# Kernel tuning notes

Measured on AMD Instinct MI355X. Metric: run time of the kernel, lower is better.

Reference implementation:

```python
import jax, jax.numpy as jnp
import numpy as np


def setup_inputs() -> dict:
    key = jax.random.key(0)
    k1, k2, k3, k4 = jax.random.split(key, 4)
    B, N, D, P = 1, 8192, 128, 2  # batch must be 1 (see .view(B,N,N) in source)
    x = jax.random.normal(k1, (B, N, D), dtype=jnp.float32)
    points = jax.random.normal(k2, (B, N, P), dtype=jnp.float32)
    # nn.Linear params, stored as (in, out) so y = x @ W + b
    W1 = jax.random.normal(k3, (2 * D, 2 * D), dtype=jnp.float32) * 0.04
    b1 = jnp.zeros((2 * D,), dtype=jnp.float32)
    W2 = jax.random.normal(k4, (2 * D, D), dtype=jnp.float32) * 0.04
    b2 = jnp.zeros((D,), dtype=jnp.float32)
    return {"x": x, "points": points, "W1": W1, "b1": b1, "W2": W2, "b2": b2, "K": 16}


def reference(x, points, W1, b1, W2, b2, K):
    B, N, _ = points.shape
    D = x.shape[-1]
    # torch.cdist on flattened (B*N, P) points, reshaped to (B, N, N)
    # (valid only for B == 1, matching the original module). Squared distance
    # is monotone in Euclidean distance, so top-k indices are identical.
    pf = points.reshape(B * N, -1)
    sq = jnp.sum(pf * pf, axis=-1)
    d2 = sq[:, None] + sq[None, :] - 2.0 * (pf @ pf.T)  # (BN, BN)
    d2 = d2.reshape(B, N, N)
    # topk(-dist, K+1) -> nearest K+1 (self first), drop self
    _, idx = jax.lax.top_k(-d2, K + 1)  # (B, N, K+1)
    idx = idx[:, :, 1:]  # (B, N, K)
    # gather neighbor features: knn_fts[b, n, k] = x[b, idx[b, n, k]]
    knn = x[jnp.arange(B)[:, None, None], idx]  # (B, N, K, D)
    center = jnp.broadcast_to(x[:, :, None, :], (B, N, K, D))
    local = jnp.concatenate([knn - center, center], axis=-1)  # (B, N, K, 2D)
    h = jax.nn.gelu(local @ W1 + b1, approximate=False)
    h = jax.nn.gelu(h @ W2 + b2, approximate=False)
    return jnp.mean(h, axis=2)  # (B, N, D)
```

## Files before the change

kernel.cpp:

```cpp
#include <hip/hip_runtime.h>

typedef __attribute__((ext_vector_type(8))) short short8;
typedef __attribute__((ext_vector_type(4))) float f32x4;

__device__ __forceinline__ unsigned short f2bf(float f) {
    unsigned int u = __float_as_uint(f);
    unsigned int r = u + 0x7fffu + ((u >> 16) & 1u);
    return (unsigned short)(r >> 16);
}

__device__ __forceinline__ float bf2f(short s) {
    return __uint_as_float(((unsigned int)(unsigned short)s) << 16);
}

__device__ __forceinline__ float gelu_fast(float v) {
    float x2 = v * v;
    float s  = v * fmaf(-0.102943195f, x2, -2.3022077f);
    float e  = __builtin_amdgcn_exp2f(s);
    return v * __builtin_amdgcn_rcpf(1.0f + e);
}

__device__ __forceinline__ unsigned int d2key(float d2) {
    unsigned int u = __float_as_uint(d2);
    return u ^ (((unsigned int)(((int)u) >> 31)) | 0x80000000u);
}

#define U64MAX 0xFFFFFFFFFFFFFFFFull

#define D2_FROM_Q(px, py, XI, YI, SQI)                                           \
    ({ const float sqj_ = __fadd_rn(__fmul_rn((px), (px)), __fmul_rn((py), (py))); \
       const float t_   = fmaf((YI), (py), __fmul_rn((XI), (px)));                 \
       const float s_   = __fadd_rn((SQI), sqj_);                                  \
       fmaf(-2.0f, t_, s_); })

__device__ __forceinline__ unsigned long long bitonic64(unsigned long long v, int lane) {
#pragma unroll
    for (int k = 2; k <= 64; k <<= 1) {
#pragma unroll
        for (int j = k >> 1; j > 0; j >>= 1) {
            unsigned long long pv = __shfl_xor(v, j, 64);
            const bool up  = ((lane & k) == 0);
            const bool low = ((lane & j) == 0);
            const unsigned long long mn = (v < pv) ? v : pv;
            const unsigned long long mx = (v < pv) ? pv : v;
            v = (up == low) ? mn : mx;
        }
    }
    return v;
}

__device__ __forceinline__ float bitonic64f(float v, int lane) {
#pragma unroll
    for (int k = 2; k <= 64; k <<= 1) {
#pragma unroll
        for (int j = k >> 1; j > 0; j >>= 1) {
            float pv = __shfl_xor(v, j, 64);
            const bool up  = ((lane & k) == 0);
            const bool low = ((lane & j) == 0);
            const float mn = fminf(v, pv);
            const float mx = fmaxf(v, pv);
            v = (up == low) ? mn : mx;
        }
    }
    return v;
}

__device__ __forceinline__ void insert_cand(
        unsigned long long* crow, int* cnt,
        float px, float py, float XI, float YI, float SQI, int i) {
    const float d2 = D2_FROM_Q(px, py, XI, YI, SQI);
    const unsigned int key = d2key(d2);
    int pos = atomicAdd(cnt, 1);
    if (pos < 128)
        crow[pos] = ((unsigned long long)key << 32) | (unsigned int)i;
}

#define KNN_SLACK 2.0e-3f

__global__ __launch_bounds__(512) void knn_kernel(
        const float* __restrict__ points,
        const float* __restrict__ W1, const float* __restrict__ W2,
        unsigned short* __restrict__ W1t, unsigned short* __restrict__ W2t,
        int* __restrict__ idx_out) {
    __shared__ float pmin[8][8][64];
    __shared__ float tshr[8];
    __shared__ unsigned long long cand[8][128];
    __shared__ int ccnt[8];

    const int bid = blockIdx.x;
    const int tid = threadIdx.x;

    if (bid < 192) {
        int g = bid * 512 + tid;
        if (g < 65536) {
            int d = g >> 8, c = g & 255;
            W1t[c * 256 + d] = f2bf(W1[g]);
        } else {
            int g2 = g - 65536;
            int d = g2 >> 7, c = g2 & 127;
            W2t[c * 256 + d] = f2bf(W2[g2]);
        }
        return;
    }

    const int wv    = tid >> 6;
    const int lane  = tid & 63;
    const int qbase = (bid - 192) << 3;

    float xi[8], yi[8], sqi_[8], n2x[8], n2y[8];
#pragma unroll
    for (int t = 0; t < 8; ++t) {
        xi[t] = points[(qbase + t) * 2 + 0];
        yi[t] = points[(qbase + t) * 2 + 1];
        sqi_[t] = __fadd_rn(__fmul_rn(xi[t], xi[t]), __fmul_rn(yi[t], yi[t]));
        n2x[t] = -2.0f * xi[t];
        n2y[t] = -2.0f * yi[t];
    }

    const float4* p4 = (const float4*)points;
    const float4* pw = p4 + wv * 512 + lane;

    if (tid < 8) ccnt[tid] = 0;

    float vmn[8] = {1e30f, 1e30f, 1e30f, 1e30f, 1e30f, 1e30f, 1e30f, 1e30f};
#pragma unroll
    for (int j = 0; j < 8; ++j) {
        const float4 pp = pw[j * 64];
        const float sqa = fmaf(pp.x, pp.x, pp.y * pp.y);
        const float sqb = fmaf(pp.z, pp.z, pp.w * pp.w);
#pragma unroll
        for (int t = 0; t < 8; ++t) {
            const float da = fmaf(n2x[t], pp.x, fmaf(n2y[t], pp.y, sqa));
            const float db = fmaf(n2x[t], pp.z, fmaf(n2y[t], pp.w, sqb));
            vmn[t] = fminf(fminf(da, db), vmn[t]);
        }
    }
#pragma unroll
    for (int t = 0; t < 8; ++t) pmin[t][wv][lane] = vmn[t];
    __syncthreads();

    {
        float m = pmin[wv][0][lane];
#pragma unroll
        for (int w = 1; w < 8; ++w) m = fminf(m, pmin[wv][w][lane]);
        const float s = bitonic64f(m, lane);
        if (lane == 16) tshr[wv] = s + KNN_SLACK;
    }
    __syncthreads();
    float Ta[8];
#pragma unroll
    for (int t = 0; t < 8; ++t) Ta[t] = tshr[t];

#pragma unroll
    for (int j = 0; j < 8; ++j) {
        const float4 pp = pw[j * 64];
        const int i0 = (wv * 512 + j * 64 + lane) * 2;
        const float sqa = fmaf(pp.x, pp.x, pp.y * pp.y);
        const float sqb = fmaf(pp.z, pp.z, pp.w * pp.w);
#pragma unroll
        for (int t = 0; t < 8; ++t) {
            const float da = fmaf(n2x[t], pp.x, fmaf(n2y[t], pp.y, sqa));
            const float db = fmaf(n2x[t], pp.z, fmaf(n2y[t], pp.w, sqb));
            if (da <= Ta[t])
                insert_cand(cand[t], &ccnt[t],
                            pp.x, pp.y, xi[t], yi[t], sqi_[t], i0);
            if (db <= Ta[t])
                insert_cand(cand[t], &ccnt[t],
                            pp.z, pp.w, xi[t], yi[t], sqi_[t], i0 + 1);
        }
    }
    __syncthreads();

    {
        const int q = qbase + wv;
        unsigned long long* candw = cand[wv];
        const int cc = ccnt[wv];
        const int n = cc < 128 ? cc : 128;
        if (n <= 64) {
            unsigned long long v0 = (lane < n) ? candw[lane] : U64MAX;
            v0 = bitonic64(v0, lane);
            if (lane >= 1 && lane <= 16)
                idx_out[q * 16 + lane - 1] = (int)(unsigned int)(v0 & 0xFFFFFFFFull);
        } else {
            unsigned long long v0 = (lane < n)      ? candw[lane]      : U64MAX;
            unsigned long long v1 = (lane + 64 < n) ? candw[lane + 64] : U64MAX;
#pragma unroll 1
            for (int pick = 0; pick < 17; ++pick) {
                unsigned long long m = (v0 < v1) ? v0 : v1;
#pragma unroll
                for (int d = 1; d < 64; d <<= 1) {
                    unsigned long long pm = __shfl_xor(m, d, 64);
                    m = (pm < m) ? pm : m;
                }
                if (pick > 0 && lane == 0)
                    idx_out[q * 16 + pick - 1] = (int)(unsigned int)(m & 0xFFFFFFFFull);
                if (v0 == m) v0 = U64MAX;
                else if (v1 == m) v1 = U64MAX;
            }
        }
    }
}

__global__ __launch_bounds__(256) void gemmAD_kernel(
        const float* __restrict__ x, const unsigned short* __restrict__ W1t,
        const float* __restrict__ b1,
        unsigned short* __restrict__ Abf, unsigned short* __restrict__ Dbf) {
    __shared__ unsigned short sx[64 * 136];
    __shared__ unsigned short tA[64 * 68];
    __shared__ unsigned short tD[64 * 68];
    const int tid = threadIdx.x;
    const int rb  = (blockIdx.x >> 2) * 64;
    const int cb  = (blockIdx.x & 3) * 64;

    {
        const int r   = ((tid >> 6) << 4) | (tid & 15);
        const int seg = (tid >> 4) & 3;
        const float* xr = x + (rb + r) * 128 + seg * 32;
        unsigned short* dst = sx + r * 136 + seg * 32;
#pragma unroll
        for (int u = 0; u < 8; ++u) {
            float4 a = ((const float4*)xr)[u];
            uint2 w;
            w.x = (unsigned)f2bf(a.x) | ((unsigned)f2bf(a.y) << 16);
            w.y = (unsigned)f2bf(a.z) | ((unsigned)f2bf(a.w) << 16);
            *(uint2*)(dst + u * 4) = w;
        }
    }
    __syncthreads();

    const int lane = tid & 63, wv = tid >> 6;
    const int m = lane & 15, quad = lane >> 4;
    const int ko0 = quad * 8;

    f32x4 accA[4], accC[4];
#pragma unroll
    for (int i = 0; i < 4; ++i) { accA[i] = (f32x4){0,0,0,0}; accC[i] = (f32x4){0,0,0,0}; }

    const int colL = wv * 16 + m;

#pragma unroll
    for (int ks = 0; ks < 4; ++ks) {
        const int ko = ks * 32 + ko0;
        short8 af[4];
#pragma unroll
        for (int rt = 0; rt < 4; ++rt)
            af[rt] = *(const short8*)(sx + (rt * 16 + m) * 136 + ko);
        const unsigned short* wp = W1t + (cb + colL) * 256 + ko;
        const short8 bA = *(const short8*)(wp);
        const short8 bC = *(const short8*)(wp + 128);
#pragma unroll
        for (int rt = 0; rt < 4; ++rt) {
            accA[rt] = __builtin_amdgcn_mfma_f32_16x16x32_bf16(af[rt], bA, accA[rt], 0, 0, 0);
            accC[rt] = __builtin_amdgcn_mfma_f32_16x16x32_bf16(af[rt], bC, accC[rt], 0, 0, 0);
        }
    }

    {
        const float bias = b1[cb + colL];
#pragma unroll
        for (int rt = 0; rt < 4; ++rt)
#pragma unroll
            for (int j = 0; j < 4; ++j) {
                const int rowL = rt * 16 + quad * 4 + j;
                float a = accA[rt][j];
                float d = accC[rt][j] - a + bias;
                tA[rowL * 68 + colL] = f2bf(a);
                tD[rowL * 68 + colL] = f2bf(d);
            }
    }
    __syncthreads();

    {
        const int r  = tid >> 2;
        const int sg = tid & 3;
        const unsigned short* sa = tA + r * 68 + sg * 16;
        const unsigned short* sd = tD + r * 68 + sg * 16;
        unsigned short* da = Abf + (rb + r) * 256 + cb + sg * 16;
        unsigned short* dd = Dbf + (rb + r) * 256 + cb + sg * 16;
        *(short8*)(da)     = *(const short8*)(sa);
        *(short8*)(da + 8) = *(const short8*)(sa + 8);
        *(short8*)(dd)     = *(const short8*)(sd);
        *(short8*)(dd + 8) = *(const short8*)(sd + 8);
    }
}

__global__ __launch_bounds__(256) void mlp_kernel(
        const unsigned short* __restrict__ Abf, const unsigned short* __restrict__ Dbf,
        const unsigned short* __restrict__ W2t, const float* __restrict__ b2,
        const int* __restrict__ idx, float* __restrict__ out) {
    __shared__ unsigned short sh[64 * 264];
    const int tid = threadIdx.x;
    const int qb  = blockIdx.x << 2;

    {
        const int r   = ((tid >> 6) << 4) | (tid & 15);
        const int seg = (tid >> 4) & 3;
        const int gq  = qb + (r >> 4);
        const int nb  = idx[(gq << 4) + (r & 15)];
        const unsigned short* arow = Abf + nb * 256 + seg * 64;
        const unsigned short* drow = Dbf + gq * 256 + seg * 64;
        unsigned short* dst = sh + r * 264 + seg * 64;
#pragma unroll
        for (int u = 0; u < 8; ++u) {
            short8 av = *(const short8*)(arow + u * 8);
            short8 dv = *(const short8*)(drow + u * 8);
            short8 hv;
#pragma unroll
            for (int e = 0; e < 8; ++e) {
                float h = bf2f(av[e]) + bf2f(dv[e]);
                hv[e] = (short)f2bf(gelu_fast(h));
            }
            *(short8*)(dst + u * 8) = hv;
        }
    }
    __syncthreads();

    const int lane = tid & 63, wv = tid >> 6;
    const int m = lane & 15, quad = lane >> 4;
    const int ko0 = quad * 8;

    f32x4 acc2[8];
#pragma unroll
    for (int i = 0; i < 8; ++i) acc2[i] = (f32x4){0.f, 0.f, 0.f, 0.f};
#pragma unroll
    for (int ks = 0; ks < 8; ++ks) {
        const int ko = ks * 32 + ko0;
        short8 af[4], bfr[2];
#pragma unroll
        for (int rt = 0; rt < 4; ++rt)
            af[rt] = *(const short8*)(sh + (rt * 16 + m) * 264 + ko);
#pragma unroll
        for (int ct = 0; ct < 2; ++ct)
            bfr[ct] = *(const short8*)(W2t + (wv * 32 + ct * 16 + m) * 256 + ko);
#pragma unroll
        for (int rt = 0; rt < 4; ++rt)
#pragma unroll
            for (int ct = 0; ct < 2; ++ct)
                acc2[rt * 2 + ct] = __builtin_amdgcn_mfma_f32_16x16x32_bf16(
                    af[rt], bfr[ct], acc2[rt * 2 + ct], 0, 0, 0);
    }

#pragma unroll
    for (int ct = 0; ct < 2; ++ct) {
        const int col = wv * 32 + ct * 16 + m;
        const float bias = b2[col];
#pragma unroll
        for (int rt = 0; rt < 4; ++rt) {
            float s = 0.f;
#pragma unroll
            for (int j = 0; j < 4; ++j)
                s += gelu_fast(acc2[rt * 2 + ct][j] + bias);
            s += __shfl_xor(s, 16, 64);
            s += __shfl_xor(s, 32, 64);
            if (quad == 0) out[(qb + rt) * 128 + col] = s * 0.0625f;
        }
    }
}

extern "C" void kernel_launch(void* const* d_in, const int* in_sizes, int n_in,
                              void* d_out, int out_size, void* d_ws, size_t ws_size,
                              hipStream_t stream) {
    const float* x      = (const float*)d_in[0];
    const float* points = (const float*)d_in[1];
    const float* W1     = (const float*)d_in[2];
    const float* b1     = (const float*)d_in[3];
    const float* W2     = (const float*)d_in[4];
    const float* b2     = (const float*)d_in[5];
    float* out = (float*)d_out;

    char* ws = (char*)d_ws;
    unsigned short* W1t = (unsigned short*)ws;
    unsigned short* W2t = (unsigned short*)(ws + 131072);
    int*            idx = (int*)(ws + 196608);
    unsigned short* Abf = (unsigned short*)(ws + 720896);
    unsigned short* Dbf = (unsigned short*)(ws + 4915200);

    knn_kernel<<<1216, 512, 0, stream>>>(points, W1, W2, W1t, W2t, idx);
    gemmAD_kernel<<<512, 256, 0, stream>>>(x, W1t, b1, Abf, Dbf);
    mlp_kernel<<<2048, 256, 0, stream>>>(Abf, Dbf, W2t, b2, idx, out);
}
```

Before: 135.6 us.

## Shrink kNN blocks to four queries, use packed FMA, convert W1 in gemm

Measured after the change: 138.0 us. No clear change (+1.8%).

```diff
diff --git a/kernel.cpp b/kernel.cpp
--- a/kernel.cpp
+++ b/kernel.cpp
@@ -2,6 +2,7 @@
 
 typedef __attribute__((ext_vector_type(8))) short short8;
 typedef __attribute__((ext_vector_type(4))) float f32x4;
+typedef __attribute__((ext_vector_type(2))) float f32x2;
 
 __device__ __forceinline__ unsigned short f2bf(float f) {
     unsigned int u = __float_as_uint(f);
@@ -23,6 +24,17 @@
 __device__ __forceinline__ unsigned int d2key(float d2) {
     unsigned int u = __float_as_uint(d2);
     return u ^ (((unsigned int)(((int)u) >> 31)) | 0x80000000u);
+}
+
+__device__ __forceinline__ f32x2 pk_fma(f32x2 a, f32x2 b, f32x2 c) {
+    f32x2 d;
+    asm("v_pk_fma_f32 %0, %1, %2, %3" : "=v"(d) : "v"(a), "v"(b), "v"(c));
+    return d;
+}
+__device__ __forceinline__ f32x2 pk_mul(f32x2 a, f32x2 b) {
+    f32x2 d;
+    asm("v_pk_mul_f32 %0, %1, %2" : "=v"(d) : "v"(a), "v"(b));
+    return d;
 }
 
 #define U64MAX 0xFFFFFFFFFFFFFFFFull
@@ -77,94 +89,88 @@
 
 #define KNN_SLACK 2.0e-3f
 
-__global__ __launch_bounds__(512) void knn_kernel(
+__global__ __launch_bounds__(256) void knn_kernel(
         const float* __restrict__ points,
-        const float* __restrict__ W1, const float* __restrict__ W2,
-        unsigned short* __restrict__ W1t, unsigned short* __restrict__ W2t,
+        const float* __restrict__ W2,
+        unsigned short* __restrict__ W2t,
         int* __restrict__ idx_out) {
-    __shared__ float pmin[8][8][64];
-    __shared__ float tshr[8];
-    __shared__ unsigned long long cand[8][128];
-    __shared__ int ccnt[8];
+    __shared__ float pmin[4][4][64];
+    __shared__ float tshr[4];
+    __shared__ unsigned long long cand[4][128];
+    __shared__ int ccnt[4];
 
     const int bid = blockIdx.x;
     const int tid = threadIdx.x;
 
-    if (bid < 192) {
-        int g = bid * 512 + tid;
-        if (g < 65536) {
-            int d = g >> 8, c = g & 255;
-            W1t[c * 256 + d] = f2bf(W1[g]);
-        } else {
-            int g2 = g - 65536;
-            int d = g2 >> 7, c = g2 & 127;
-            W2t[c * 256 + d] = f2bf(W2[g2]);
-        }
+    if (bid < 128) {
+        int g = bid * 256 + tid;
+        int d = g >> 7, c = g & 127;
+        W2t[c * 256 + d] = f2bf(W2[g]);
         return;
     }
 
     const int wv    = tid >> 6;
     const int lane  = tid & 63;
-    const int qbase = (bid - 192) << 3;
-
-    float xi[8], yi[8], sqi_[8], n2x[8], n2y[8];
-#pragma unroll
-    for (int t = 0; t < 8; ++t) {
+    const int qbase = (bid - 128) << 2;
+
+    float xi[4], yi[4], sqi_[4];
+    f32x2 n2x2[4], n2y2[4];
+#pragma unroll
+    for (int t = 0; t < 4; ++t) {
         xi[t] = points[(qbase + t) * 2 + 0];
         yi[t] = points[(qbase + t) * 2 + 1];
         sqi_[t] = __fadd_rn(__fmul_rn(xi[t], xi[t]), __fmul_rn(yi[t], yi[t]));
-        n2x[t] = -2.0f * xi[t];
-        n2y[t] = -2.0f * yi[t];
+        const float nx = -2.0f * xi[t], ny = -2.0f * yi[t];
+        n2x2[t] = (f32x2){nx, nx};
+        n2y2[t] = (f32x2){ny, ny};
     }
 
     const float4* p4 = (const float4*)points;
-    const float4* pw = p4 + wv * 512 + lane;
-
-    if (tid < 8) ccnt[tid] = 0;
-
-    float vmn[8] = {1e30f, 1e30f, 1e30f, 1e30f, 1e30f, 1e30f, 1e30f, 1e30f};
-#pragma unroll
-    for (int j = 0; j < 8; ++j) {
+    const float4* pw = p4 + wv * 1024 + lane;
+
+    if (tid < 4) ccnt[tid] = 0;
+
+    float vmn[4] = {1e30f, 1e30f, 1e30f, 1e30f};
+#pragma unroll 4
+    for (int j = 0; j < 16; ++j) {
         const float4 pp = pw[j * 64];
-        const float sqa = fmaf(pp.x, pp.x, pp.y * pp.y);
-        const float sqb = fmaf(pp.z, pp.z, pp.w * pp.w);
-#pragma unroll
-        for (int t = 0; t < 8; ++t) {
-            const float da = fmaf(n2x[t], pp.x, fmaf(n2y[t], pp.y, sqa));
-            const float db = fmaf(n2x[t], pp.z, fmaf(n2y[t], pp.w, sqb));
-            vmn[t] = fminf(fminf(da, db), vmn[t]);
-        }
-    }
-#pragma unroll
-    for (int t = 0; t < 8; ++t) pmin[t][wv][lane] = vmn[t];
-    __syncthreads();
-
-    {
-        float m = pmin[wv][0][lane];
-#pragma unroll
-        for (int w = 1; w < 8; ++w) m = fminf(m, pmin[wv][w][lane]);
+        const f32x2 pxz = {pp.x, pp.z}, pyw = {pp.y, pp.w};
+        const f32x2 sq2 = pk_fma(pxz, pxz, pk_mul(pyw, pyw));
+#pragma unroll
+        for (int t = 0; t < 4; ++t) {
+            const f32x2 d2 = pk_fma(n2x2[t], pxz, pk_fma(n2y2[t], pyw, sq2));
+            vmn[t] = fminf(fminf(d2.x, d2.y), vmn[t]);
+        }
+    }
+#pragma unroll
+    for (int t = 0; t < 4; ++t) pmin[t][wv][lane] = vmn[t];
+    __syncthreads();
+
+    {
+        const int q = wv;
+        const float m = fminf(fminf(pmin[q][0][lane], pmin[q][1][lane]),
+                              fminf(pmin[q][2][lane], pmin[q][3][lane]));
         const float s = bitonic64f(m, lane);
-        if (lane == 16) tshr[wv] = s + KNN_SLACK;
-    }
-    __syncthreads();
-    float Ta[8];
-#pragma unroll
-    for (int t = 0; t < 8; ++t) Ta[t] = tshr[t];
-
-#pragma unroll
-    for (int j = 0; j < 8; ++j) {
+        if (lane == 16) tshr[q] = s + KNN_SLACK;
+    }
+    __syncthreads();
+    float Ta[4];
+#pragma unroll
+    for (int t = 0; t < 4; ++t) Ta[t] = tshr[t];
+
+#pragma unroll 4
+    for (int j = 0; j < 16; ++j) {
         const float4 pp = pw[j * 64];
-        const int i0 = (wv * 512 + j * 64 + lane) * 2;
-        const float sqa = fmaf(pp.x, pp.x, pp.y * pp.y);
-        const float sqb = fmaf(pp.z, pp.z, pp.w * pp.w);
-#pragma unroll
-        for (int t = 0; t < 8; ++t) {
-            const float da = fmaf(n2x[t], pp.x, fmaf(n2y[t], pp.y, sqa));
-            const float db = fmaf(n2x[t], pp.z, fmaf(n2y[t], pp.w, sqb));
-            if (da <= Ta[t])
+        const int i0 = (wv * 1024 + j * 64 + lane) * 2;
+        const f32x2 pxz = {pp.x, pp.z}, pyw = {pp.y, pp.w};
+        const f32x2 sq2 = pk_fma(pxz, pxz, pk_mul(pyw, pyw));
+#pragma unroll
+        for (int t = 0; t < 4; ++t) {
+            const f32x2 d2 = pk_fma(n2x2[t], pxz, pk_fma(n2y2[t], pyw, sq2));
+            if (d2.x <= Ta[t])
                 insert_cand(cand[t], &ccnt[t],
                             pp.x, pp.y, xi[t], yi[t], sqi_[t], i0);
-            if (db <= Ta[t])
+            if (d2.y <= Ta[t])
                 insert_cand(cand[t], &ccnt[t],
                             pp.z, pp.w, xi[t], yi[t], sqi_[t], i0 + 1);
         }
@@ -202,7 +208,7 @@
 }
 
 __global__ __launch_bounds__(256) void gemmAD_kernel(
-        const float* __restrict__ x, const unsigned short* __restrict__ W1t,
+        const float* __restrict__ x, const float* __restrict__ W1,
         const float* __restrict__ b1,
         unsigned short* __restrict__ Abf, unsigned short* __restrict__ Dbf) {
     __shared__ unsigned short sx[64 * 136];
@@ -237,6 +243,7 @@
     for (int i = 0; i < 4; ++i) { accA[i] = (f32x4){0,0,0,0}; accC[i] = (f32x4){0,0,0,0}; }
 
     const int colL = wv * 16 + m;
+    const int gc   = cb + colL;
 
 #pragma unroll
     for (int ks = 0; ks < 4; ++ks) {
@@ -245,9 +252,12 @@
 #pragma unroll
         for (int rt = 0; rt < 4; ++rt)
             af[rt] = *(const short8*)(sx + (rt * 16 + m) * 136 + ko);
-        const unsigned short* wp = W1t + (cb + colL) * 256 + ko;
-        const short8 bA = *(const short8*)(wp);
-        const short8 bC = *(const short8*)(wp + 128);
+        short8 bA, bC;
+#pragma unroll
+        for (int e = 0; e < 8; ++e) {
+            bA[e] = (short)f2bf(W1[(ko + e) * 256 + gc]);
+            bC[e] = (short)f2bf(W1[(128 + ko + e) * 256 + gc]);
+        }
 #pragma unroll
         for (int rt = 0; rt < 4; ++rt) {
             accA[rt] = __builtin_amdgcn_mfma_f32_16x16x32_bf16(af[rt], bA, accA[rt], 0, 0, 0);
@@ -256,7 +266,7 @@
     }
 
     {
-        const float bias = b1[cb + colL];
+        const float bias = b1[gc];
 #pragma unroll
         for (int rt = 0; rt < 4; ++rt)
 #pragma unroll
@@ -369,13 +379,12 @@
     float* out = (float*)d_out;
 
     char* ws = (char*)d_ws;
-    unsigned short* W1t = (unsigned short*)ws;
     unsigned short* W2t = (unsigned short*)(ws + 131072);
     int*            idx = (int*)(ws + 196608);
     unsigned short* Abf = (unsigned short*)(ws + 720896);
     unsigned short* Dbf = (unsigned short*)(ws + 4915200);
 
-    knn_kernel<<<1216, 512, 0, stream>>>(points, W1, W2, W1t, W2t, idx);
-    gemmAD_kernel<<<512, 256, 0, stream>>>(x, W1t, b1, Abf, Dbf);
+    knn_kernel<<<2176, 256, 0, stream>>>(points, W2, W2t, idx);
+    gemmAD_kernel<<<512, 256, 0, stream>>>(x, W1, b1, Abf, Dbf);
     mlp_kernel<<<2048, 256, 0, stream>>>(Abf, Dbf, W2t, b2, idx, out);
 }
```
